# Kernel tuning notes

Measured on AMD Instinct MI355X. Metric: run time of the kernel, lower is better.

## Reference

```python
import jax, jax.numpy as jnp
import numpy as np

HEADS = 8
DIM_HEAD = 64
LN_EPS = 1e-5


def _layernorm(x, gamma, beta):
    # LayerNorm over last axis (dim_head), torch default eps=1e-5, biased variance
    mu = jnp.mean(x, axis=-1, keepdims=True)
    var = jnp.mean(jnp.square(x - mu), axis=-1, keepdims=True)
    return (x - mu) * jax.lax.rsqrt(var + LN_EPS) * gamma + beta


def setup_inputs() -> dict:
    key = jax.random.key(0)
    k1, k2 = jax.random.split(key)
    B, L, W, C = 8, 64, 64, 512
    inner = HEADS * DIM_HEAD  # 512
    x = jax.random.normal(k1, (B, L, W, C), dtype=jnp.float32)
    # nn.Linear(dim, 3*inner, bias=False); stored as [in, out] for x @ w
    w_qkv = jax.random.normal(k2, (C, 3 * inner), dtype=jnp.float32) * 0.02
    q_gamma = jnp.ones((DIM_HEAD,), dtype=jnp.float32)
    q_beta = jnp.zeros((DIM_HEAD,), dtype=jnp.float32)
    k_gamma = jnp.ones((DIM_HEAD,), dtype=jnp.float32)
    k_beta = jnp.zeros((DIM_HEAD,), dtype=jnp.float32)
    return {"x": x, "w_qkv": w_qkv, "q_gamma": q_gamma, "q_beta": q_beta,
            "k_gamma": k_gamma, "k_beta": k_beta}


def reference(x, w_qkv, q_gamma, q_beta, k_gamma, k_beta):
    B, L, W, C = x.shape
    n = L * W
    xf = x.reshape(B, n, C)                          # [B, N, C]
    qkv = xf @ w_qkv                                 # [B, N, 3*inner]
    q, k, v = jnp.split(qkv, 3, axis=-1)             # each [B, N, inner]

    def to_heads(t):
        # b n (h d) -> b h n d
        return t.reshape(B, n, HEADS, DIM_HEAD).transpose(0, 2, 1, 3)

    q, k, v = to_heads(q), to_heads(k), to_heads(v)
    q = _layernorm(q, q_gamma, q_beta)
    k = _layernorm(k, k_gamma, k_beta)

    dots = jnp.einsum('bhnd,bhne->bhde', k, v)       # K^T V : [B,H,d,d]
    out = jnp.einsum('bhnd,bhde->bhne', q, dots) * (1.0 / n)  # [B,H,N,d]
    # b h n d -> b n (h d) -> b L W (h d)
    out = out.transpose(0, 2, 1, 3).reshape(B, L, W, HEADS * DIM_HEAD)
    return out
```

## Files before the change

### kernel.cpp

```cpp
#include <hip/hip_runtime.h>
#include <hip/hip_bf16.h>
#include <stdint.h>

typedef __bf16 bf16;
typedef __bf16 bf16x8 __attribute__((ext_vector_type(8)));
typedef __bf16 bf16x4 __attribute__((ext_vector_type(4)));
typedef float  f32x4  __attribute__((ext_vector_type(4)));
typedef unsigned int u32;

typedef __attribute__((address_space(1))) u32 gu32;
typedef __attribute__((address_space(3))) u32 lu32;

__device__ __forceinline__ void gld_lds16(const void* g, void* l) {
  __builtin_amdgcn_global_load_lds((gu32*)(uintptr_t)g, (lu32*)(u32)(uintptr_t)l, 16, 0, 0);
}

__device__ __forceinline__ f32x4 mfma_bf16_16x16x32(bf16x8 a, bf16x8 b, f32x4 c) {
  return __builtin_amdgcn_mfma_f32_16x16x32_bf16(a, b, c, 0, 0, 0);
}

#define LGKM0 do { asm volatile("s_waitcnt lgkmcnt(0)" ::: "memory"); \
                   __builtin_amdgcn_sched_barrier(0); } while (0)
#define VMC(n) do { asm volatile("s_waitcnt vmcnt(" #n ")" ::: "memory"); } while (0)
#define BAR __builtin_amdgcn_s_barrier()
#define PRIO1 __builtin_amdgcn_s_setprio(1)
#define PRIO0 __builtin_amdgcn_s_setprio(0)

__global__ __launch_bounds__(256) void k_cast_x(const float* __restrict__ x,
                                                bf16* __restrict__ xb) {
  size_t i = (size_t)blockIdx.x * 256 + threadIdx.x;
  const float4* p = (const float4*)x + i * 2;
  float4 a = p[0], b = p[1];
  bf16x8 o;
  o[0] = (bf16)a.x; o[1] = (bf16)a.y; o[2] = (bf16)a.z; o[3] = (bf16)a.w;
  o[4] = (bf16)b.x; o[5] = (bf16)b.y; o[6] = (bf16)b.z; o[7] = (bf16)b.w;
  *(bf16x8*)(xb + i * 8) = o;
}

__global__ __launch_bounds__(256) void k_prep_w(const float* __restrict__ w,
                                                bf16* __restrict__ wT) {
  int idx = blockIdx.x * 256 + threadIdx.x;
  int r = idx >> 9;
  int k = idx & 511;
  int c;
  if (r < 512) {
    c = r;
  } else {
    int rr = r - 512;
    int hp = rr >> 8;
    int q2 = (rr >> 6) & 3;
    int d = r & 63;
    int h = 2 * hp + (q2 & 1);
    c = ((q2 < 2) ? 512 : 1024) + h * 64 + d;
  }
  wT[idx] = (bf16)w[k * 1536 + c];
}

template <int MH, int NH>
__device__ __forceinline__ void mm(f32x4 (&acc)[8][4],
                                   const bf16x8 (&a)[4][2],
                                   const bf16x8 (&b)[2][2]) {
#pragma unroll
  for (int fm = 0; fm < 4; ++fm)
#pragma unroll
    for (int fn = 0; fn < 2; ++fn)
#pragma unroll
      for (int ks = 0; ks < 2; ++ks)
        acc[MH * 4 + fm][NH * 2 + fn] =
            mfma_bf16_16x16x32(a[fm][ks], b[fn][ks], acc[MH * 4 + fm][NH * 2 + fn]);
}

__global__ __launch_bounds__(512, 2) void k_qkv_gemm(
    const bf16* __restrict__ A, const bf16* __restrict__ Bt,
    const float* __restrict__ qg, const float* __restrict__ qbeta,
    const float* __restrict__ kg, const float* __restrict__ kbeta,
    bf16* __restrict__ qh, float* __restrict__ dTp)
{
  extern __shared__ bf16 lds[];
  const int tid = threadIdx.x;
  const int lane = tid & 63;
  const int w = tid >> 6;
  const int wm = w >> 2;
  const int wn = w & 3;

  const int wg = blockIdx.x;
  const int swz = (wg & 7) * 96 + (wg >> 3);
  const int tn = swz % 6;
  const int tm = swz / 6;

  auto stA = [&](int buf, int slot, int ktile) {
#pragma unroll
    for (int i = 0; i < 2; ++i) {
      int vr = i * 64 + w * 8 + (lane >> 3);
      int grow = tm * 256 + (vr >> 6) * 128 + slot * 64 + (vr & 63);
      int gk = ktile * 64 + (((lane & 7) ^ (vr & 7)) * 8);
      gld_lds16(A + (size_t)grow * 512 + gk,
                (char*)lds + (buf * 2 + slot) * 16384 + i * 8192 + w * 1024);
    }
  };
  auto stB = [&](int buf, int slot, int ktile) {
#pragma unroll
    for (int i = 0; i < 2; ++i) {
      int vr = i * 64 + w * 8 + (lane >> 3);
      int grow = tn * 256 + (vr >> 5) * 64 + slot * 32 + (vr & 31);
      int gk = ktile * 64 + (((lane & 7) ^ (vr & 7)) * 8);
      gld_lds16(Bt + (size_t)grow * 512 + gk,
                (char*)lds + 65536 + (buf * 2 + slot) * 16384 + i * 8192 + w * 1024);
    }
  };
  auto rdA = [&](int buf, int mh, bf16x8 (&fr)[4][2]) {
    const bf16* base = lds + (buf * 2 + mh) * 8192;
#pragma unroll
    for (int f = 0; f < 4; ++f) {
      int vr = wm * 64 + f * 16 + (lane & 15);
#pragma unroll
      for (int ks = 0; ks < 2; ++ks) {
        int pb = (ks * 4 + (lane >> 4)) ^ (vr & 7);
        fr[f][ks] = *(const bf16x8*)(base + vr * 64 + pb * 8);
      }
    }
  };
  auto rdB = [&](int buf, int nh, bf16x8 (&fr)[2][2]) {
    const bf16* base = lds + 32768 + (buf * 2 + nh) * 8192;
#pragma unroll
    for (int f = 0; f < 2; ++f) {
      int vr = wn * 32 + f * 16 + (lane & 15);
#pragma unroll
      for (int ks = 0; ks < 2; ++ks) {
        int pb = (ks * 4 + (lane >> 4)) ^ (vr & 7);
        fr[f][ks] = *(const bf16x8*)(base + vr * 64 + pb * 8);
      }
    }
  };

  bf16x8 afr[4][2];
  bf16x8 bfr[2][2][2];
  f32x4 acc[8][4];
  {
    f32x4 z = {0.f, 0.f, 0.f, 0.f};
#pragma unroll
    for (int m = 0; m < 8; ++m)
#pragma unroll
      for (int n = 0; n < 4; ++n) acc[m][n] = z;
  }

  stA(0, 0, 0); stB(0, 0, 0); stA(0, 1, 0); stB(0, 1, 0);
  stA(1, 0, 1); stB(1, 0, 1); stA(1, 1, 1); stB(1, 1, 1);
  asm volatile("s_waitcnt vmcnt(8)" ::: "memory");
  BAR;

  for (int t = 0; t < 8; ++t) {
    const int d = t & 1;
    rdA(d, 0, afr);
    rdB(d, 0, bfr[0]);
    if (t >= 1 && t <= 6) stA(d ^ 1, 1, t + 1);
    BAR;
    LGKM0;
    PRIO1; mm<0, 0>(acc, afr, bfr[0]); PRIO0;
    BAR;

    rdB(d, 1, bfr[1]);
    if (t >= 1 && t <= 6) stB(d ^ 1, 1, t + 1);
    BAR;
    LGKM0;
    PRIO1; mm<0, 1>(acc, afr, bfr[1]); PRIO0;
    BAR;

    rdA(d, 1, afr);
    if (t <= 5) stA(d, 0, t + 2);
    BAR;
    LGKM0;
    PRIO1; mm<1, 0>(acc, afr, bfr[0]); PRIO0;
    BAR;

    if (t <= 5) stB(d, 0, t + 2);
    BAR;
    PRIO1; mm<1, 1>(acc, afr, bfr[1]); PRIO0;
    if (t < 6) { VMC(4); } else if (t == 6) { VMC(0); }
    BAR;
  }

  const int dlane = lane & 15;
  const int rsub = (lane >> 4) * 4;

  if (tn < 2) {
    const int hcol = tn * 4 + wn;
    float g4[4], b4[4];
#pragma unroll
    for (int fn = 0; fn < 4; ++fn) {
      g4[fn] = qg[fn * 16 + dlane];
      b4[fn] = qbeta[fn * 16 + dlane];
    }
#pragma unroll
    for (int m = 0; m < 8; ++m) {
      float mu[4], rs[4];
#pragma unroll
      for (int r = 0; r < 4; ++r) {
        float s  = acc[m][0][r] + acc[m][1][r] + acc[m][2][r] + acc[m][3][r];
        float s2 = acc[m][0][r] * acc[m][0][r] + acc[m][1][r] * acc[m][1][r]
                 + acc[m][2][r] * acc[m][2][r] + acc[m][3][r] * acc[m][3][r];
#pragma unroll
        for (int msk = 1; msk < 16; msk <<= 1) {
          s  += __shfl_xor(s, msk, 64);
          s2 += __shfl_xor(s2, msk, 64);
        }
        float mean = s * (1.0f / 64.0f);
        float var  = s2 * (1.0f / 64.0f) - mean * mean;
        mu[r] = mean;
        rs[r] = rsqrtf(var + 1e-5f);
      }
      int rowg = tm * 256 + wm * 128 + m * 16 + rsub;
      int bb = rowg >> 12, n0 = rowg & 4095;
      int bh = bb * 8 + hcol;
      bf16* dst = qh + ((size_t)bh * 4096 + n0) * 64;
#pragma unroll
      for (int r = 0; r < 4; ++r)
#pragma unroll
        for (int fn = 0; fn < 4; ++fn) {
          float xv = (acc[m][fn][r] - mu[r]) * rs[r] * g4[fn] + b4[fn];
          dst[(size_t)r * 64 + fn * 16 + dlane] = (bf16)xv;
        }
    }
  } else {
    const int hp = tn - 2;
    const bool isK = (wn < 2);
    const int hloc = wn & 1;
    char* reg = (char*)lds + ((isK ? 0 : 2) + hloc) * 32768;
    float g4[4], b4[4];
    if (isK) {
#pragma unroll
      for (int fn = 0; fn < 4; ++fn) {
        g4[fn] = kg[fn * 16 + dlane];
        b4[fn] = kbeta[fn * 16 + dlane];
      }
    }
#pragma unroll
    for (int m = 0; m < 8; ++m) {
      float mu[4] = {}, rs[4] = {};
      if (isK) {
#pragma unroll
        for (int r = 0; r < 4; ++r) {
          float s  = acc[m][0][r] + acc[m][1][r] + acc[m][2][r] + acc[m][3][r];
          float s2 = acc[m][0][r] * acc[m][0][r] + acc[m][1][r] * acc[m][1][r]
                   + acc[m][2][r] * acc[m][2][r] + acc[m][3][r] * acc[m][3][r];
#pragma unroll
          for (int msk = 1; msk < 16; msk <<= 1) {
            s  += __shfl_xor(s, msk, 64);
            s2 += __shfl_xor(s2, msk, 64);
          }
          float mean = s * (1.0f / 64.0f);
          float var  = s2 * (1.0f / 64.0f) - mean * mean;
          mu[r] = mean;
          rs[r] = rsqrtf(var + 1e-5f);
        }
      }
      int n0 = wm * 128 + m * 16 + rsub;
#pragma unroll
      for (int fn = 0; fn < 4; ++fn) {
        int dd = fn * 16 + dlane;
        bf16x4 pk;
#pragma unroll
        for (int r = 0; r < 4; ++r) {
          float xv = isK ? ((acc[m][fn][r] - mu[r]) * rs[r] * g4[fn] + b4[fn])
                         : acc[m][fn][r];
          pk[r] = (bf16)xv;
        }
        int blk = (n0 >> 2) ^ ((dd & 7) << 1);
        *(bf16x4*)(reg + dd * 512 + blk * 8) = pk;
      }
    }
    LGKM0;
    BAR;
    const int hsel = w >> 2;
    const int qd = w & 3;
    const char* Abase = (char*)lds + (2 + hsel) * 32768;
    const char* Bbase = (char*)lds + hsel * 32768;
    f32x4 dacc[4] = {};
#pragma unroll
    for (int t8 = 0; t8 < 8; ++t8) {
      int blkb = t8 * 8 + (lane >> 4) * 2;
      int rA = qd * 16 + dlane;
      bf16x8 va = *(const bf16x8*)(Abase + rA * 512 + (blkb ^ ((rA & 7) << 1)) * 8);
#pragma unroll
      for (int j = 0; j < 4; ++j) {
        int rB = j * 16 + dlane;
        bf16x8 vb = *(const bf16x8*)(Bbase + rB * 512 + (blkb ^ ((rB & 7) << 1)) * 8);
        dacc[j] = mfma_bf16_16x16x32(va, vb, dacc[j]);
      }
    }
    int bh = (tm >> 4) * 8 + 2 * hp + hsel;
    float* outp = dTp + ((size_t)bh * 16 + (tm & 15)) * 4096;
#pragma unroll
    for (int j = 0; j < 4; ++j)
#pragma unroll
      for (int r = 0; r < 4; ++r) {
        int e = qd * 16 + (lane >> 4) * 4 + r;
        outp[e * 64 + j * 16 + dlane] = dacc[j][r];
      }
  }
}

__global__ __launch_bounds__(256) void k_cvt_dt(const float* __restrict__ dTp,
                                                bf16* __restrict__ dTb) {
  int j = blockIdx.x * 256 + threadIdx.x;
  int bh = j >> 12;
  int i = j & 4095;
  const float* p = dTp + (size_t)bh * 65536 + i;
  float s = 0.f;
#pragma unroll
  for (int c = 0; c < 16; ++c) s += p[c * 4096];
  dTb[j] = (bf16)s;
}

__global__ __launch_bounds__(256) void k_out(const bf16* __restrict__ qh,
                                             const bf16* __restrict__ dTb,
                                             float* __restrict__ out) {
  __shared__ bf16 lA[128 * 64];
  const int tid = threadIdx.x, lane = tid & 63, w = tid >> 6;
  const int wm = w >> 1, wn = w & 1;
  const int bh = blockIdx.y, mt = blockIdx.x;
  const int bb = bh >> 3, h = bh & 7;
  const bf16* Ab = qh + (size_t)bh * 4096 * 64 + (size_t)mt * 128 * 64;
  const int srow = lane >> 3, sblk = (lane & 7) ^ srow;
#pragma unroll
  for (int i = 0; i < 4; ++i) {
    int slot = w * 4 + i;
    int row = slot * 8 + srow;
    gld_lds16(Ab + (size_t)row * 64 + sblk * 8, (char*)lA + slot * 1024);
  }
  __syncthreads();
  const bf16* Bb = dTb + (size_t)bh * 4096;
  f32x4 acc[4][2] = {};
#pragma unroll
  for (int ks = 0; ks < 2; ++ks) {
    bf16x8 af[4], bq[2];
#pragma unroll
    for (int f = 0; f < 4; ++f) {
      int row = wm * 64 + f * 16 + (lane & 15);
      int sb = (ks * 4 + (lane >> 4)) ^ (row & 7);
      af[f] = *(const bf16x8*)(lA + row * 64 + sb * 8);
    }
#pragma unroll
    for (int fn = 0; fn < 2; ++fn) {
      int e = wn * 32 + fn * 16 + (lane & 15);
      bq[fn] = *(const bf16x8*)(Bb + e * 64 + ks * 32 + (lane >> 4) * 8);
    }
#pragma unroll
    for (int fm = 0; fm < 4; ++fm)
#pragma unroll
      for (int fn = 0; fn < 2; ++fn)
        acc[fm][fn] = mfma_bf16_16x16x32(af[fm], bq[fn], acc[fm][fn]);
  }
#pragma unroll
  for (int fm = 0; fm < 4; ++fm)
#pragma unroll
    for (int fn = 0; fn < 2; ++fn)
#pragma unroll
      for (int r = 0; r < 4; ++r) {
        int n = mt * 128 + wm * 64 + fm * 16 + (lane >> 4) * 4 + r;
        int e = wn * 32 + fn * 16 + (lane & 15);
        out[((size_t)bb * 4096 + n) * 512 + h * 64 + e] = acc[fm][fn][r] * (1.0f / 4096.0f);
      }
}

extern "C" void kernel_launch(void* const* d_in, const int* in_sizes, int n_in,
                              void* d_out, int out_size, void* d_ws, size_t ws_size,
                              hipStream_t stream) {
  const float* x  = (const float*)d_in[0];
  const float* wq = (const float*)d_in[1];
  const float* qg = (const float*)d_in[2];
  const float* qb = (const float*)d_in[3];
  const float* kg = (const float*)d_in[4];
  const float* kb = (const float*)d_in[5];
  float* out = (float*)d_out;
  char* ws = (char*)d_ws;

  bf16* xb  = (bf16*)(ws);
  bf16* wT  = (bf16*)(ws + ((size_t)32 << 20));
  bf16* qh  = (bf16*)(ws + ((size_t)34 << 20));
  float* dTp = (float*)(ws + ((size_t)66 << 20));
  bf16* dTb  = (bf16*)(ws + ((size_t)83 << 20));

  k_cast_x<<<8192, 256, 0, stream>>>(x, xb);
  k_prep_w<<<3072, 256, 0, stream>>>(wq, wT);
  k_qkv_gemm<<<768, 512, 131072, stream>>>(xb, wT, qg, qb, kg, kb, qh, dTp);
  k_cvt_dt<<<1024, 256, 0, stream>>>(dTp, dTb);
  k_out<<<dim3(32, 64), 256, 0, stream>>>(qh, dTb, out);
}
```

Before: 112.8 us.

## Load GEMM B operand directly from global to registers and halve LDS

The QKV GEMM no longer stages the weight (B) tile through LDS. Each wave loads its B fragments straight from global memory into registers and double-buffers them across k-tiles. The A pipeline is restructured to two phases per k-tile, and the K^T V epilogue now runs in two rounds, one per head, so the same LDS region can be reused. Together these cut dynamic LDS from 128KB to 64KB, which could allow two blocks per CU. The cost is more registers, uncoalesced global B reads that lean on cache, and an extra barrier round in the epilogue.

After: 161.8 us. 1.43x slower.

```diff
diff --git a/kernel.cpp b/kernel.cpp
--- a/kernel.cpp
+++ b/kernel.cpp
@@ -95,21 +95,11 @@
       int grow = tm * 256 + (vr >> 6) * 128 + slot * 64 + (vr & 63);
       int gk = ktile * 64 + (((lane & 7) ^ (vr & 7)) * 8);
       gld_lds16(A + (size_t)grow * 512 + gk,
-                (char*)lds + (buf * 2 + slot) * 16384 + i * 8192 + w * 1024);
-    }
-  };
-  auto stB = [&](int buf, int slot, int ktile) {
-#pragma unroll
-    for (int i = 0; i < 2; ++i) {
-      int vr = i * 64 + w * 8 + (lane >> 3);
-      int grow = tn * 256 + (vr >> 5) * 64 + slot * 32 + (vr & 31);
-      int gk = ktile * 64 + (((lane & 7) ^ (vr & 7)) * 8);
-      gld_lds16(Bt + (size_t)grow * 512 + gk,
-                (char*)lds + 65536 + (buf * 2 + slot) * 16384 + i * 8192 + w * 1024);
+                (char*)lds + buf * 32768 + slot * 16384 + i * 8192 + w * 1024);
     }
   };
   auto rdA = [&](int buf, int mh, bf16x8 (&fr)[4][2]) {
-    const bf16* base = lds + (buf * 2 + mh) * 8192;
+    const bf16* base = lds + buf * 16384 + mh * 8192;
 #pragma unroll
     for (int f = 0; f < 4; ++f) {
       int vr = wm * 64 + f * 16 + (lane & 15);
@@ -120,21 +110,21 @@
       }
     }
   };
-  auto rdB = [&](int buf, int nh, bf16x8 (&fr)[2][2]) {
-    const bf16* base = lds + 32768 + (buf * 2 + nh) * 8192;
-#pragma unroll
-    for (int f = 0; f < 2; ++f) {
-      int vr = wn * 32 + f * 16 + (lane & 15);
-#pragma unroll
-      for (int ks = 0; ks < 2; ++ks) {
-        int pb = (ks * 4 + (lane >> 4)) ^ (vr & 7);
-        fr[f][ks] = *(const bf16x8*)(base + vr * 64 + pb * 8);
-      }
-    }
+  const bf16* bbase = Bt + ((size_t)(tn * 256 + wn * 64) + (lane & 15)) * 512
+                         + (lane >> 4) * 8;
+  auto loadB = [&](bf16x8 (&bb)[2][2][2], int t) {
+#pragma unroll
+    for (int nh = 0; nh < 2; ++nh)
+#pragma unroll
+      for (int f = 0; f < 2; ++f)
+#pragma unroll
+        for (int ks = 0; ks < 2; ++ks)
+          bb[nh][f][ks] = *(const bf16x8*)(bbase + (size_t)(nh * 32 + f * 16) * 512
+                                                 + t * 64 + ks * 32);
   };
 
   bf16x8 afr[4][2];
-  bf16x8 bfr[2][2][2];
+  bf16x8 bc[2][2][2], bn[2][2][2];
   f32x4 acc[8][4];
   {
     f32x4 z = {0.f, 0.f, 0.f, 0.f};
@@ -144,40 +134,35 @@
       for (int n = 0; n < 4; ++n) acc[m][n] = z;
   }
 
-  stA(0, 0, 0); stB(0, 0, 0); stA(0, 1, 0); stB(0, 1, 0);
-  stA(1, 0, 1); stB(1, 0, 1); stA(1, 1, 1); stB(1, 1, 1);
-  asm volatile("s_waitcnt vmcnt(8)" ::: "memory");
+  stA(0, 0, 0); stA(0, 1, 0);
+  loadB(bc, 0);
+  VMC(8);
   BAR;
 
+#pragma unroll
   for (int t = 0; t < 8; ++t) {
     const int d = t & 1;
     rdA(d, 0, afr);
-    rdB(d, 0, bfr[0]);
-    if (t >= 1 && t <= 6) stA(d ^ 1, 1, t + 1);
+    if (t < 7) stA(d ^ 1, 0, t + 1);
     BAR;
     LGKM0;
-    PRIO1; mm<0, 0>(acc, afr, bfr[0]); PRIO0;
+    PRIO1; mm<0, 0>(acc, afr, bc[0]); mm<0, 1>(acc, afr, bc[1]); PRIO0;
     BAR;
-
-    rdB(d, 1, bfr[1]);
-    if (t >= 1 && t <= 6) stB(d ^ 1, 1, t + 1);
+    rdA(d, 1, afr);
+    if (t < 7) { stA(d ^ 1, 1, t + 1); loadB(bn, t + 1); }
     BAR;
     LGKM0;
-    PRIO1; mm<0, 1>(acc, afr, bfr[1]); PRIO0;
+    PRIO1; mm<1, 0>(acc, afr, bc[0]); mm<1, 1>(acc, afr, bc[1]); PRIO0;
+    if (t < 7) VMC(8);
     BAR;
-
-    rdA(d, 1, afr);
-    if (t <= 5) stA(d, 0, t + 2);
-    BAR;
-    LGKM0;
-    PRIO1; mm<1, 0>(acc, afr, bfr[0]); PRIO0;
-    BAR;
-
-    if (t <= 5) stB(d, 0, t + 2);
-    BAR;
-    PRIO1; mm<1, 1>(acc, afr, bfr[1]); PRIO0;
-    if (t < 6) { VMC(4); } else if (t == 6) { VMC(0); }
-    BAR;
+    if (t < 7) {
+#pragma unroll
+      for (int nh = 0; nh < 2; ++nh)
+#pragma unroll
+        for (int f = 0; f < 2; ++f)
+#pragma unroll
+          for (int ks = 0; ks < 2; ++ks) bc[nh][f][ks] = bn[nh][f][ks];
+    }
   }
 
   const int dlane = lane & 15;
@@ -210,8 +195,8 @@
         rs[r] = rsqrtf(var + 1e-5f);
       }
       int rowg = tm * 256 + wm * 128 + m * 16 + rsub;
-      int bb = rowg >> 12, n0 = rowg & 4095;
-      int bh = bb * 8 + hcol;
+      int bb2 = rowg >> 12, n0 = rowg & 4095;
+      int bh = bb2 * 8 + hcol;
       bf16* dst = qh + ((size_t)bh * 4096 + n0) * 64;
 #pragma unroll
       for (int r = 0; r < 4; ++r)
@@ -225,7 +210,7 @@
     const int hp = tn - 2;
     const bool isK = (wn < 2);
     const int hloc = wn & 1;
-    char* reg = (char*)lds + ((isK ? 0 : 2) + hloc) * 32768;
+    char* reg = (char*)lds + (isK ? 0 : 32768);
     float g4[4], b4[4];
     if (isK) {
 #pragma unroll
@@ -234,69 +219,75 @@
         b4[fn] = kbeta[fn * 16 + dlane];
       }
     }
-#pragma unroll
-    for (int m = 0; m < 8; ++m) {
-      float mu[4] = {}, rs[4] = {};
-      if (isK) {
+    const int qd = w & 3;
+    const int jh = w >> 2;
+#pragma unroll
+    for (int rnd = 0; rnd < 2; ++rnd) {
+      if (hloc == rnd) {
+#pragma unroll
+        for (int m = 0; m < 8; ++m) {
+          float mu[4] = {}, rs[4] = {};
+          if (isK) {
+#pragma unroll
+            for (int r = 0; r < 4; ++r) {
+              float s  = acc[m][0][r] + acc[m][1][r] + acc[m][2][r] + acc[m][3][r];
+              float s2 = acc[m][0][r] * acc[m][0][r] + acc[m][1][r] * acc[m][1][r]
+                       + acc[m][2][r] * acc[m][2][r] + acc[m][3][r] * acc[m][3][r];
+#pragma unroll
+              for (int msk = 1; msk < 16; msk <<= 1) {
+                s  += __shfl_xor(s, msk, 64);
+                s2 += __shfl_xor(s2, msk, 64);
+              }
+              float mean = s * (1.0f / 64.0f);
+              float var  = s2 * (1.0f / 64.0f) - mean * mean;
+              mu[r] = mean;
+              rs[r] = rsqrtf(var + 1e-5f);
+            }
+          }
+          int n0 = wm * 128 + m * 16 + rsub;
+#pragma unroll
+          for (int fn = 0; fn < 4; ++fn) {
+            int dd = fn * 16 + dlane;
+            bf16x4 pk;
+#pragma unroll
+            for (int r = 0; r < 4; ++r) {
+              float xv = isK ? ((acc[m][fn][r] - mu[r]) * rs[r] * g4[fn] + b4[fn])
+                             : acc[m][fn][r];
+              pk[r] = (bf16)xv;
+            }
+            int blk = (n0 >> 2) ^ ((dd & 7) << 1);
+            *(bf16x4*)(reg + dd * 512 + blk * 8) = pk;
+          }
+        }
+      }
+      LGKM0;
+      BAR;
+      const char* Abase = (char*)lds + 32768;
+      const char* Bbase = (char*)lds;
+      f32x4 dacc[2] = {};
+#pragma unroll
+      for (int t8 = 0; t8 < 8; ++t8) {
+        int blkb = t8 * 8 + (lane >> 4) * 2;
+        int rA = qd * 16 + dlane;
+        bf16x8 va = *(const bf16x8*)(Abase + rA * 512 + (blkb ^ ((rA & 7) << 1)) * 8);
+#pragma unroll
+        for (int j = 0; j < 2; ++j) {
+          int rB = jh * 32 + j * 16 + dlane;
+          bf16x8 vb = *(const bf16x8*)(Bbase + rB * 512 + (blkb ^ ((rB & 7) << 1)) * 8);
+          dacc[j] = mfma_bf16_16x16x32(va, vb, dacc[j]);
+        }
+      }
+      int bh = (tm >> 4) * 8 + 2 * hp + rnd;
+      float* outp = dTp + ((size_t)bh * 16 + (tm & 15)) * 4096;
+#pragma unroll
+      for (int j = 0; j < 2; ++j)
 #pragma unroll
         for (int r = 0; r < 4; ++r) {
-          float s  = acc[m][0][r] + acc[m][1][r] + acc[m][2][r] + acc[m][3][r];
-          float s2 = acc[m][0][r] * acc[m][0][r] + acc[m][1][r] * acc[m][1][r]
-                   + acc[m][2][r] * acc[m][2][r] + acc[m][3][r] * acc[m][3][r];
-#pragma unroll
-          for (int msk = 1; msk < 16; msk <<= 1) {
-            s  += __shfl_xor(s, msk, 64);
-            s2 += __shfl_xor(s2, msk, 64);
-          }
-          float mean = s * (1.0f / 64.0f);
-          float var  = s2 * (1.0f / 64.0f) - mean * mean;
-          mu[r] = mean;
-          rs[r] = rsqrtf(var + 1e-5f);
-        }
-      }
-      int n0 = wm * 128 + m * 16 + rsub;
-#pragma unroll
-      for (int fn = 0; fn < 4; ++fn) {
-        int dd = fn * 16 + dlane;
-        bf16x4 pk;
-#pragma unroll
-        for (int r = 0; r < 4; ++r) {
-          float xv = isK ? ((acc[m][fn][r] - mu[r]) * rs[r] * g4[fn] + b4[fn])
-                         : acc[m][fn][r];
-          pk[r] = (bf16)xv;
-        }
-        int blk = (n0 >> 2) ^ ((dd & 7) << 1);
-        *(bf16x4*)(reg + dd * 512 + blk * 8) = pk;
-      }
-    }
-    LGKM0;
-    BAR;
-    const int hsel = w >> 2;
-    const int qd = w & 3;
-    const char* Abase = (char*)lds + (2 + hsel) * 32768;
-    const char* Bbase = (char*)lds + hsel * 32768;
-    f32x4 dacc[4] = {};
-#pragma unroll
-    for (int t8 = 0; t8 < 8; ++t8) {
-      int blkb = t8 * 8 + (lane >> 4) * 2;
-      int rA = qd * 16 + dlane;
-      bf16x8 va = *(const bf16x8*)(Abase + rA * 512 + (blkb ^ ((rA & 7) << 1)) * 8);
-#pragma unroll
-      for (int j = 0; j < 4; ++j) {
-        int rB = j * 16 + dlane;
-        bf16x8 vb = *(const bf16x8*)(Bbase + rB * 512 + (blkb ^ ((rB & 7) << 1)) * 8);
-        dacc[j] = mfma_bf16_16x16x32(va, vb, dacc[j]);
-      }
-    }
-    int bh = (tm >> 4) * 8 + 2 * hp + hsel;
-    float* outp = dTp + ((size_t)bh * 16 + (tm & 15)) * 4096;
-#pragma unroll
-    for (int j = 0; j < 4; ++j)
-#pragma unroll
-      for (int r = 0; r < 4; ++r) {
-        int e = qd * 16 + (lane >> 4) * 4 + r;
-        outp[e * 64 + j * 16 + dlane] = dacc[j][r];
-      }
+          int e = qd * 16 + (lane >> 4) * 4 + r;
+          outp[e * 64 + jh * 32 + j * 16 + dlane] = dacc[j][r];
+        }
+      if (rnd == 0) { LGKM0; BAR; }
+    }
   }
 }
 
@@ -383,7 +374,7 @@
 
   k_cast_x<<<8192, 256, 0, stream>>>(x, xb);
   k_prep_w<<<3072, 256, 0, stream>>>(wq, wT);
-  k_qkv_gemm<<<768, 512, 131072, stream>>>(xb, wT, qg, qb, kg, kb, qh, dTp);
+  k_qkv_gemm<<<768, 512, 65536, stream>>>(xb, wT, qg, qb, kg, kb, qh, dTp);
   k_cvt_dt<<<1024, 256, 0, stream>>>(dTp, dTb);
   k_out<<<dim3(32, 64), 256, 0, stream>>>(qh, dTb, out);
 }
```

## Shrink QKV GEMM tile to 128x128 with 4 waves and simple double buffering

Applied to the files above, without the earlier changes.

The QKV GEMM moves from 256x256 tiles with 8 waves and a hand-interleaved four-phase pipeline with priority hints to 128x128 tiles with 4 waves and a plain double-buffered loop. The weight column permutation and the fused K^T V epilogue are reworked to the smaller tile, so each block now produces one head's partial d x d product. That doubles the partial-sum count that k_cvt_dt has to reduce. The change trades operand reuse per tile and the fine-grained load/compute overlap for more blocks, lower LDS use and simpler scheduling.

Result: slower. 123.7 us (+9.7%).

```diff
diff --git a/kernel.cpp b/kernel.cpp
--- a/kernel.cpp
+++ b/kernel.cpp
@@ -21,10 +21,8 @@
 
 #define LGKM0 do { asm volatile("s_waitcnt lgkmcnt(0)" ::: "memory"); \
                    __builtin_amdgcn_sched_barrier(0); } while (0)
-#define VMC(n) do { asm volatile("s_waitcnt vmcnt(" #n ")" ::: "memory"); } while (0)
+#define VMC0 do { asm volatile("s_waitcnt vmcnt(0)" ::: "memory"); } while (0)
 #define BAR __builtin_amdgcn_s_barrier()
-#define PRIO1 __builtin_amdgcn_s_setprio(1)
-#define PRIO0 __builtin_amdgcn_s_setprio(0)
 
 __global__ __launch_bounds__(256) void k_cast_x(const float* __restrict__ x,
                                                 bf16* __restrict__ xb) {
@@ -47,30 +45,15 @@
     c = r;
   } else {
     int rr = r - 512;
-    int hp = rr >> 8;
-    int q2 = (rr >> 6) & 3;
+    int h = rr >> 7;
+    int half = (rr >> 6) & 1;
     int d = r & 63;
-    int h = 2 * hp + (q2 & 1);
-    c = ((q2 < 2) ? 512 : 1024) + h * 64 + d;
+    c = (half == 0 ? 512 : 1024) + h * 64 + d;
   }
   wT[idx] = (bf16)w[k * 1536 + c];
 }
 
-template <int MH, int NH>
-__device__ __forceinline__ void mm(f32x4 (&acc)[8][4],
-                                   const bf16x8 (&a)[4][2],
-                                   const bf16x8 (&b)[2][2]) {
-#pragma unroll
-  for (int fm = 0; fm < 4; ++fm)
-#pragma unroll
-    for (int fn = 0; fn < 2; ++fn)
-#pragma unroll
-      for (int ks = 0; ks < 2; ++ks)
-        acc[MH * 4 + fm][NH * 2 + fn] =
-            mfma_bf16_16x16x32(a[fm][ks], b[fn][ks], acc[MH * 4 + fm][NH * 2 + fn]);
-}
-
-__global__ __launch_bounds__(512, 2) void k_qkv_gemm(
+__global__ __launch_bounds__(256, 2) void k_qkv_gemm(
     const bf16* __restrict__ A, const bf16* __restrict__ Bt,
     const float* __restrict__ qg, const float* __restrict__ qbeta,
     const float* __restrict__ kg, const float* __restrict__ kbeta,
@@ -80,36 +63,34 @@
   const int tid = threadIdx.x;
   const int lane = tid & 63;
   const int w = tid >> 6;
-  const int wm = w >> 2;
-  const int wn = w & 3;
+  const int wm = w >> 1;
+  const int wn = w & 1;
 
   const int wg = blockIdx.x;
-  const int swz = (wg & 7) * 96 + (wg >> 3);
-  const int tn = swz % 6;
-  const int tm = swz / 6;
-
-  auto stA = [&](int buf, int slot, int ktile) {
-#pragma unroll
-    for (int i = 0; i < 2; ++i) {
-      int vr = i * 64 + w * 8 + (lane >> 3);
-      int grow = tm * 256 + (vr >> 6) * 128 + slot * 64 + (vr & 63);
+  const int swz = (wg & 7) * 384 + (wg >> 3);
+  const int tn = swz % 12;
+  const int tm = swz / 12;
+
+  auto stA = [&](int buf, int ktile) {
+#pragma unroll
+    for (int i = 0; i < 4; ++i) {
+      int vr = i * 32 + w * 8 + (lane >> 3);
       int gk = ktile * 64 + (((lane & 7) ^ (vr & 7)) * 8);
-      gld_lds16(A + (size_t)grow * 512 + gk,
-                (char*)lds + (buf * 2 + slot) * 16384 + i * 8192 + w * 1024);
+      gld_lds16(A + (size_t)(tm * 128 + vr) * 512 + gk,
+                (char*)lds + buf * 16384 + i * 4096 + w * 1024);
     }
   };
-  auto stB = [&](int buf, int slot, int ktile) {
-#pragma unroll
-    for (int i = 0; i < 2; ++i) {
-      int vr = i * 64 + w * 8 + (lane >> 3);
-      int grow = tn * 256 + (vr >> 5) * 64 + slot * 32 + (vr & 31);
+  auto stB = [&](int buf, int ktile) {
+#pragma unroll
+    for (int i = 0; i < 4; ++i) {
+      int vr = i * 32 + w * 8 + (lane >> 3);
       int gk = ktile * 64 + (((lane & 7) ^ (vr & 7)) * 8);
-      gld_lds16(Bt + (size_t)grow * 512 + gk,
-                (char*)lds + 65536 + (buf * 2 + slot) * 16384 + i * 8192 + w * 1024);
+      gld_lds16(Bt + (size_t)(tn * 128 + vr) * 512 + gk,
+                (char*)lds + 32768 + buf * 16384 + i * 4096 + w * 1024);
     }
   };
-  auto rdA = [&](int buf, int mh, bf16x8 (&fr)[4][2]) {
-    const bf16* base = lds + (buf * 2 + mh) * 8192;
+  auto rdA = [&](int buf, bf16x8 (&fr)[4][2]) {
+    const bf16* base = lds + buf * 8192;
 #pragma unroll
     for (int f = 0; f < 4; ++f) {
       int vr = wm * 64 + f * 16 + (lane & 15);
@@ -120,11 +101,11 @@
       }
     }
   };
-  auto rdB = [&](int buf, int nh, bf16x8 (&fr)[2][2]) {
-    const bf16* base = lds + 32768 + (buf * 2 + nh) * 8192;
-#pragma unroll
-    for (int f = 0; f < 2; ++f) {
-      int vr = wn * 32 + f * 16 + (lane & 15);
+  auto rdB = [&](int buf, bf16x8 (&fr)[4][2]) {
+    const bf16* base = lds + 16384 + buf * 8192;
+#pragma unroll
+    for (int f = 0; f < 4; ++f) {
+      int vr = wn * 64 + f * 16 + (lane & 15);
 #pragma unroll
       for (int ks = 0; ks < 2; ++ks) {
         int pb = (ks * 4 + (lane >> 4)) ^ (vr & 7);
@@ -133,58 +114,40 @@
     }
   };
 
-  bf16x8 afr[4][2];
-  bf16x8 bfr[2][2][2];
-  f32x4 acc[8][4];
+  bf16x8 af[4][2], bf[4][2];
+  f32x4 acc[4][4];
   {
     f32x4 z = {0.f, 0.f, 0.f, 0.f};
 #pragma unroll
-    for (int m = 0; m < 8; ++m)
+    for (int m = 0; m < 4; ++m)
 #pragma unroll
       for (int n = 0; n < 4; ++n) acc[m][n] = z;
   }
 
-  stA(0, 0, 0); stB(0, 0, 0); stA(0, 1, 0); stB(0, 1, 0);
-  stA(1, 0, 1); stB(1, 0, 1); stA(1, 1, 1); stB(1, 1, 1);
-  asm volatile("s_waitcnt vmcnt(8)" ::: "memory");
-  BAR;
-
+  stA(0, 0); stB(0, 0);
+  VMC0; BAR;
+
+#pragma unroll
   for (int t = 0; t < 8; ++t) {
     const int d = t & 1;
-    rdA(d, 0, afr);
-    rdB(d, 0, bfr[0]);
-    if (t >= 1 && t <= 6) stA(d ^ 1, 1, t + 1);
-    BAR;
-    LGKM0;
-    PRIO1; mm<0, 0>(acc, afr, bfr[0]); PRIO0;
-    BAR;
-
-    rdB(d, 1, bfr[1]);
-    if (t >= 1 && t <= 6) stB(d ^ 1, 1, t + 1);
-    BAR;
-    LGKM0;
-    PRIO1; mm<0, 1>(acc, afr, bfr[1]); PRIO0;
-    BAR;
-
-    rdA(d, 1, afr);
-    if (t <= 5) stA(d, 0, t + 2);
-    BAR;
-    LGKM0;
-    PRIO1; mm<1, 0>(acc, afr, bfr[0]); PRIO0;
-    BAR;
-
-    if (t <= 5) stB(d, 0, t + 2);
-    BAR;
-    PRIO1; mm<1, 1>(acc, afr, bfr[1]); PRIO0;
-    if (t < 6) { VMC(4); } else if (t == 6) { VMC(0); }
+    if (t < 7) { stA(d ^ 1, t + 1); stB(d ^ 1, t + 1); }
+    rdA(d, af); rdB(d, bf);
+#pragma unroll
+    for (int fm = 0; fm < 4; ++fm)
+#pragma unroll
+      for (int fn = 0; fn < 4; ++fn)
+#pragma unroll
+        for (int ks = 0; ks < 2; ++ks)
+          acc[fm][fn] = mfma_bf16_16x16x32(af[fm][ks], bf[fn][ks], acc[fm][fn]);
+    if (t < 7) VMC0;
     BAR;
   }
 
   const int dlane = lane & 15;
   const int rsub = (lane >> 4) * 4;
 
-  if (tn < 2) {
-    const int hcol = tn * 4 + wn;
+  if (tn < 4) {
+    const int hcol = tn * 2 + wn;
     float g4[4], b4[4];
 #pragma unroll
     for (int fn = 0; fn < 4; ++fn) {
@@ -192,7 +155,7 @@
       b4[fn] = qbeta[fn * 16 + dlane];
     }
 #pragma unroll
-    for (int m = 0; m < 8; ++m) {
+    for (int m = 0; m < 4; ++m) {
       float mu[4], rs[4];
 #pragma unroll
       for (int r = 0; r < 4; ++r) {
@@ -209,9 +172,9 @@
         mu[r] = mean;
         rs[r] = rsqrtf(var + 1e-5f);
       }
-      int rowg = tm * 256 + wm * 128 + m * 16 + rsub;
-      int bb = rowg >> 12, n0 = rowg & 4095;
-      int bh = bb * 8 + hcol;
+      int rowg = tm * 128 + wm * 64 + m * 16 + rsub;
+      int bb2 = rowg >> 12, n0 = rowg & 4095;
+      int bh = bb2 * 8 + hcol;
       bf16* dst = qh + ((size_t)bh * 4096 + n0) * 64;
 #pragma unroll
       for (int r = 0; r < 4; ++r)
@@ -222,10 +185,9 @@
         }
     }
   } else {
-    const int hp = tn - 2;
-    const bool isK = (wn < 2);
-    const int hloc = wn & 1;
-    char* reg = (char*)lds + ((isK ? 0 : 2) + hloc) * 32768;
+    const int h = tn - 4;
+    const bool isK = (wn == 0);
+    char* reg = (char*)lds + (isK ? 0 : 16384);
     float g4[4], b4[4];
     if (isK) {
 #pragma unroll
@@ -235,7 +197,7 @@
       }
     }
 #pragma unroll
-    for (int m = 0; m < 8; ++m) {
+    for (int m = 0; m < 4; ++m) {
       float mu[4] = {}, rs[4] = {};
       if (isK) {
 #pragma unroll
@@ -254,7 +216,7 @@
           rs[r] = rsqrtf(var + 1e-5f);
         }
       }
-      int n0 = wm * 128 + m * 16 + rsub;
+      int n0 = wm * 64 + m * 16 + rsub;
 #pragma unroll
       for (int fn = 0; fn < 4; ++fn) {
         int dd = fn * 16 + dlane;
@@ -266,30 +228,29 @@
           pk[r] = (bf16)xv;
         }
         int blk = (n0 >> 2) ^ ((dd & 7) << 1);
-        *(bf16x4*)(reg + dd * 512 + blk * 8) = pk;
+        *(bf16x4*)(reg + dd * 256 + blk * 8) = pk;
       }
     }
     LGKM0;
     BAR;
-    const int hsel = w >> 2;
-    const int qd = w & 3;
-    const char* Abase = (char*)lds + (2 + hsel) * 32768;
-    const char* Bbase = (char*)lds + hsel * 32768;
+    const int qd = w;
+    const char* vT = (char*)lds + 16384;
+    const char* kT = (char*)lds;
     f32x4 dacc[4] = {};
 #pragma unroll
-    for (int t8 = 0; t8 < 8; ++t8) {
-      int blkb = t8 * 8 + (lane >> 4) * 2;
-      int rA = qd * 16 + dlane;
-      bf16x8 va = *(const bf16x8*)(Abase + rA * 512 + (blkb ^ ((rA & 7) << 1)) * 8);
+    for (int ks = 0; ks < 4; ++ks) {
+      int g0 = ks * 8 + (lane >> 4) * 2;
+      int e = qd * 16 + dlane;
+      bf16x8 va = *(const bf16x8*)(vT + e * 256 + (g0 ^ ((e & 7) << 1)) * 8);
 #pragma unroll
       for (int j = 0; j < 4; ++j) {
-        int rB = j * 16 + dlane;
-        bf16x8 vb = *(const bf16x8*)(Bbase + rB * 512 + (blkb ^ ((rB & 7) << 1)) * 8);
+        int dk = j * 16 + dlane;
+        bf16x8 vb = *(const bf16x8*)(kT + dk * 256 + (g0 ^ ((dk & 7) << 1)) * 8);
         dacc[j] = mfma_bf16_16x16x32(va, vb, dacc[j]);
       }
     }
-    int bh = (tm >> 4) * 8 + 2 * hp + hsel;
-    float* outp = dTp + ((size_t)bh * 16 + (tm & 15)) * 4096;
+    int bh = (tm >> 5) * 8 + h;
+    float* outp = dTp + ((size_t)bh * 32 + (tm & 31)) * 4096;
 #pragma unroll
     for (int j = 0; j < 4; ++j)
 #pragma unroll
@@ -305,10 +266,10 @@
   int j = blockIdx.x * 256 + threadIdx.x;
   int bh = j >> 12;
   int i = j & 4095;
-  const float* p = dTp + (size_t)bh * 65536 + i;
+  const float* p = dTp + (size_t)bh * 131072 + i;
   float s = 0.f;
 #pragma unroll
-  for (int c = 0; c < 16; ++c) s += p[c * 4096];
+  for (int c = 0; c < 32; ++c) s += p[c * 4096];
   dTb[j] = (bf16)s;
 }
 
@@ -379,11 +340,11 @@
   bf16* wT  = (bf16*)(ws + ((size_t)32 << 20));
   bf16* qh  = (bf16*)(ws + ((size_t)34 << 20));
   float* dTp = (float*)(ws + ((size_t)66 << 20));
-  bf16* dTb  = (bf16*)(ws + ((size_t)83 << 20));
+  bf16* dTb  = (bf16*)(ws + ((size_t)99 << 20));
 
   k_cast_x<<<8192, 256, 0, stream>>>(x, xb);
   k_prep_w<<<3072, 256, 0, stream>>>(wq, wT);
-  k_qkv_gemm<<<768, 512, 131072, stream>>>(xb, wT, qg, qb, kg, kb, qh, dTp);
+  k_qkv_gemm<<<3072, 256, 65536, stream>>>(xb, wT, qg, qb, kg, kb, qh, dTp);
   k_cvt_dt<<<1024, 256, 0, stream>>>(dTp, dTb);
   k_out<<<dim3(32, 64), 256, 0, stream>>>(qh, dTb, out);
 }
```
